# Kernel tuning notes

Measured on AMD Instinct MI355X. Metric: run time of the kernel, lower is better.

Reference implementation:

```python
import jax, jax.numpy as jnp
import numpy as np

NHEADS = 16
HEAD_DIM = 64
HIDDEN = 1024
QKV = NHEADS * HEAD_DIM  # 1024
SCALING = HEAD_DIM ** -0.5


def setup_inputs() -> dict:
    key = jax.random.key(0)
    k1, k2, k3, k4, k5 = jax.random.split(key, 5)
    B, S = 2, 2048
    hidden_states = jax.random.normal(k1, (B, S, HIDDEN), dtype=jnp.float32)
    # nn.Linear weights: stored [out, in]; kaiming-uniform-ish init scale
    w_qkv = jax.random.normal(k2, (3 * QKV, HIDDEN), dtype=jnp.float32) * (HIDDEN ** -0.5)
    b_qkv = jax.random.normal(k3, (3 * QKV,), dtype=jnp.float32) * 0.01
    w_o = jax.random.normal(k4, (HIDDEN, QKV), dtype=jnp.float32) * (QKV ** -0.5)
    b_o = jax.random.normal(k5, (HIDDEN,), dtype=jnp.float32) * 0.01
    return {"hidden_states": hidden_states, "w_qkv": w_qkv, "b_qkv": b_qkv,
            "w_o": w_o, "b_o": b_o}


def reference(hidden_states, w_qkv, b_qkv, w_o, b_o):
    B, S, _ = hidden_states.shape
    # qkv projection: x @ W^T + b  (torch nn.Linear convention)
    qkv = jnp.einsum('bsh,oh->bso', hidden_states, w_qkv) + b_qkv  # [B,S,3*QKV]
    xq, xk, xv = jnp.split(qkv, 3, axis=-1)
    # [B,S,H,D] -> [B,H,S,D]
    q = xq.reshape(B, S, NHEADS, HEAD_DIM).transpose(0, 2, 1, 3)
    k = xk.reshape(B, S, NHEADS, HEAD_DIM).transpose(0, 2, 1, 3)
    v = xv.reshape(B, S, NHEADS, HEAD_DIM).transpose(0, 2, 1, 3)
    scores = jnp.einsum('bhqd,bhkd->bhqk', q, k) * SCALING
    # dropout is identity in eval mode; mask is None in this config
    probs = jax.nn.softmax(scores.astype(jnp.float32), axis=-1).astype(q.dtype)
    out = jnp.einsum('bhqk,bhkd->bhqd', probs, v)  # [B,H,S,D]
    out = out.transpose(0, 2, 1, 3).reshape(B, S, QKV)
    return jnp.einsum('bsq,oq->bso', out, w_o) + b_o
```

## Files before the change

### kernel.cpp

```cpp
#include <hip/hip_runtime.h>

#define SEQ     2048
#define MROWS   4096
#define HID     1024
#define QKV3    3072
#define NH      16
#define HD      64
#define QSCALE  0.18033688f

typedef unsigned short u16;
typedef unsigned int   u32;
typedef __attribute__((ext_vector_type(8)))  short  bf16x8;
typedef __attribute__((ext_vector_type(4)))  float  floatx4;
typedef __attribute__((ext_vector_type(16))) float  floatx16;

__device__ __forceinline__ u16 f2bf(float f) {
    u32 u = __builtin_bit_cast(u32, f);
    u += 0x7fffu + ((u >> 16) & 1u);
    return (u16)(u >> 16);
}

#if __has_builtin(__builtin_amdgcn_cvt_pk_bf16_f32)
__device__ __forceinline__ ushort2 pack_bf(float a, float b) {
    auto r = __builtin_amdgcn_cvt_pk_bf16_f32(a, b);
    return __builtin_bit_cast(ushort2, r);
}
#else
__device__ __forceinline__ ushort2 pack_bf(float a, float b) {
    u32 ua = __builtin_bit_cast(u32, a) + 0x8000u;
    u32 ub = __builtin_bit_cast(u32, b) + 0x8000u;
    u32 d  = __builtin_amdgcn_perm(ub, ua, 0x07060302u);
    return __builtin_bit_cast(ushort2, d);
}
#endif

__device__ __forceinline__ void async_cp16(const void* g, void* l) {
    __builtin_amdgcn_global_load_lds(
        (const __attribute__((address_space(1))) unsigned int*)g,
        (__attribute__((address_space(3))) unsigned int*)l, 16, 0, 0);
}

#define N4_X   (MROWS * HID / 4)
#define N4_WQ  (QKV3 * HID / 4)
#define N4_WO  (HID * HID / 4)
__global__ void cvt_all(const float* __restrict__ x, const float* __restrict__ wq,
                        const float* __restrict__ wo, u16* __restrict__ xb,
                        u16* __restrict__ wqb, u16* __restrict__ wob) {
    int i = blockIdx.x * blockDim.x + threadIdx.x;
    const float* src; u16* dst; int k;
    if (i < N4_X)                { src = x;  dst = xb;  k = i; }
    else if (i < N4_X + N4_WQ)   { src = wq; dst = wqb; k = i - N4_X; }
    else                         { src = wo; dst = wob; k = i - N4_X - N4_WQ; }
    float4 v = ((const float4*)src)[k];
    ushort2 lo = pack_bf(v.x, v.y), hi = pack_bf(v.z, v.w);
    ushort4 o = {lo.x, lo.y, hi.x, hi.y};
    ((ushort4*)dst)[k] = o;
}

template <int MODE, int NT>
__global__ __launch_bounds__(256)
void gemm_bf16_nt(const u16* __restrict__ A, const u16* __restrict__ B,
                  const float* __restrict__ bias, float* __restrict__ Cout,
                  int M, int N, int K,
                  u16* __restrict__ q_ws, u16* __restrict__ k_ws,
                  u16* __restrict__ vt_ws) {
    constexpr int WN = NT / 2;
    constexpr int NJ = WN / 16;
    __shared__ u16 As[2][128 * 32];
    __shared__ u16 Bs[2][NT * 32];
    const int t  = (int)threadIdx.x;
    const int w  = t >> 6, l = t & 63;
    const int wr = w >> 1, wc = w & 1;
    const int m0 = (int)blockIdx.y * 128, n0 = (int)blockIdx.x * NT;
    const int lrow = l >> 2;
    const int lseg = ((l & 3) ^ ((l >> 3) & 3)) * 8;
    const int fm = l & 15, fq = l >> 4;
    const int fseg = (fq ^ ((fm >> 1) & 3)) * 8;

    auto stage = [&](int k0, int bb) {
#pragma unroll
        for (int rep = 0; rep < 2; ++rep) {
            const int chunk = w + rep * 4;
            const int row   = chunk * 16 + lrow;
            async_cp16(A + (size_t)(m0 + row) * K + k0 + lseg, &As[bb][chunk * 512]);
            if (NT == 128 || rep == 0)
                async_cp16(B + (size_t)(n0 + row) * K + k0 + lseg, &Bs[bb][chunk * 512]);
        }
    };

    floatx4 acc[4][NJ];
#pragma unroll
    for (int i = 0; i < 4; ++i)
#pragma unroll
        for (int j = 0; j < NJ; ++j) acc[i][j] = (floatx4)(0.f);

    const int T = K >> 5;
    stage(0, 0);
    for (int tt = 0; tt < T; ++tt) {
        const int cur = tt & 1;
        __syncthreads();
        if (tt + 1 < T) stage((tt + 1) << 5, cur ^ 1);
        bf16x8 af[4], bf[NJ];
#pragma unroll
        for (int i = 0; i < 4; ++i)
            af[i] = *(const bf16x8*)&As[cur][(wr * 64 + i * 16 + fm) * 32 + fseg];
#pragma unroll
        for (int j = 0; j < NJ; ++j)
            bf[j] = *(const bf16x8*)&Bs[cur][(wc * WN + j * 16 + fm) * 32 + fseg];
#pragma unroll
        for (int i = 0; i < 4; ++i)
#pragma unroll
            for (int j = 0; j < NJ; ++j)
                acc[i][j] = __builtin_amdgcn_mfma_f32_16x16x32_bf16(
                    af[i], bf[j], acc[i][j], 0, 0, 0);
    }

#pragma unroll
    for (int j = 0; j < NJ; ++j) {
        const int col = n0 + wc * WN + j * 16 + fm;
        const float bv = bias[col];
        const int region = col >> 10;
        const int hh = (col >> 6) & 15, d = col & 63;
#pragma unroll
        for (int i = 0; i < 4; ++i) {
            const int row0 = m0 + wr * 64 + i * 16 + fq * 4;
            if (MODE == 0) {
#pragma unroll
                for (int r = 0; r < 4; ++r)
                    Cout[(size_t)(row0 + r) * N + col] = acc[i][j][r] + bv;
            } else if (region < 2) {
                u16* __restrict__ dst = (region == 0) ? q_ws : k_ws;
                const float sc = (region == 0) ? QSCALE : 1.0f;
#pragma unroll
                for (int r = 0; r < 4; ++r) {
                    const int row = row0 + r;
                    const int b = row >> 11, s = row & 2047;
                    dst[((size_t)(b * NH + hh) * SEQ + s) * HD + d] =
                        f2bf((acc[i][j][r] + bv) * sc);
                }
            } else {
                const int b = row0 >> 11, s0 = row0 & 2047;
                ushort2 lo = pack_bf(acc[i][j][0] + bv, acc[i][j][1] + bv);
                ushort2 hi = pack_bf(acc[i][j][2] + bv, acc[i][j][3] + bv);
                ushort4 o = {lo.x, lo.y, hi.x, hi.y};
                *(ushort4*)&vt_ws[((size_t)(b * NH + hh) * HD + d) * SEQ + s0] = o;
            }
        }
    }
}

__global__ __launch_bounds__(256)
void attn_mfma(const u16* __restrict__ qw, const u16* __restrict__ kw,
               const u16* __restrict__ vtw, u16* __restrict__ attn) {
    __shared__ u16 Ks [2][64 * 64];
    __shared__ u16 Vts[2][64 * 64];
    __shared__ u16 Ps[4][32 * 66];

    const int bh   = (int)blockIdx.x;
    const int qblk = (int)blockIdx.y * 128;
    const int t = (int)threadIdx.x;
    const int w = t >> 6, l = t & 63;
    const int ln = l & 31, half = l >> 5;
    const int srow = l >> 3, sseg = l & 7;
    const size_t headSD = (size_t)bh * SEQ * HD;
    const size_t headDS = (size_t)bh * HD * SEQ;

    auto stage = [&](int kt, int bb) {
#pragma unroll
        for (int rep = 0; rep < 2; ++rep) {
            const int c = w + rep * 4;
            async_cp16(kw + headSD + (size_t)(kt * 64 + c * 8 + srow) * HD
                           + ((sseg ^ srow) * 8), &Ks[bb][c * 512]);
            async_cp16(vtw + headDS + (size_t)(c * 8 + srow) * SEQ + kt * 64
                           + ((sseg ^ srow) * 8), &Vts[bb][c * 512]);
        }
    };

    const int qrow = qblk + w * 32 + ln;
    bf16x8 qa[4];
#pragma unroll
    for (int kc = 0; kc < 4; ++kc)
        qa[kc] = *(const bf16x8*)(qw + headSD + (size_t)qrow * HD + kc * 16 + half * 8);

    floatx16 oacc[2];
    oacc[0] = (floatx16)(0.f); oacc[1] = (floatx16)(0.f);
    float2 ps2 = {0.f, 0.f};

    stage(0, 0);
    for (int kt = 0; kt < SEQ / 64; ++kt) {
        const int cur = kt & 1;
        __syncthreads();
        if (kt + 1 < SEQ / 64) stage(kt + 1, cur ^ 1);

        floatx16 sacc[2];
        sacc[0] = (floatx16)(0.f); sacc[1] = (floatx16)(0.f);
#pragma unroll
        for (int j = 0; j < 2; ++j) {
            const int krow = j * 32 + ln;
#pragma unroll
            for (int kc = 0; kc < 4; ++kc) {
                const int seg = (2 * kc + half) ^ (krow & 7);
                bf16x8 kb = *(const bf16x8*)&Ks[cur][krow * 64 + seg * 8];
                sacc[j] = __builtin_amdgcn_mfma_f32_32x32x16_bf16(kb, qa[kc], sacc[j], 0, 0, 0);
            }
        }

#pragma unroll
        for (int j = 0; j < 2; ++j) {
#pragma unroll
            for (int g = 0; g < 4; ++g) {
#pragma unroll
                for (int rp = 0; rp < 2; ++rp) {
                    const int r0 = 4 * g + 2 * rp;
                    const float p0 = exp2f(sacc[j][r0]);
                    const float p1 = exp2f(sacc[j][r0 + 1]);
                    ps2.x += p0; ps2.y += p1;
                    *(ushort2*)&Ps[w][ln * 66 + j * 32 + 8 * g + 4 * half + 2 * rp]
                        = pack_bf(p0, p1);
                }
            }
        }

#pragma unroll
        for (int kc = 0; kc < 4; ++kc) {
            bf16x8 pb = *(const bf16x8*)&Ps[w][ln * 66 + kc * 16 + half * 8];
#pragma unroll
            for (int n = 0; n < 2; ++n) {
                const int vrow = n * 32 + ln;
                const int seg = (2 * kc + half) ^ (vrow & 7);
                bf16x8 vb = *(const bf16x8*)&Vts[cur][vrow * 64 + seg * 8];
                oacc[n] = __builtin_amdgcn_mfma_f32_32x32x16_bf16(vb, pb, oacc[n], 0, 0, 0);
            }
        }
    }

    float psum = ps2.x + ps2.y;
    const float lsum = psum + __shfl_xor(psum, 32);
    const float inv  = 1.0f / lsum;

    const int b = bh >> 4, h = bh & 15;
    u16* __restrict__ orow =
        attn + (size_t)(b * SEQ + qblk + w * 32 + ln) * HID + h * HD;
#pragma unroll
    for (int n = 0; n < 2; ++n) {
#pragma unroll
        for (int g = 0; g < 4; ++g) {
#pragma unroll
            for (int rp = 0; rp < 2; ++rp) {
                const int r0 = 4 * g + 2 * rp;
                *(ushort2*)&orow[n * 32 + 8 * g + 4 * half + 2 * rp]
                    = pack_bf(oacc[n][r0] * inv, oacc[n][r0 + 1] * inv);
            }
        }
    }
}

extern "C" void kernel_launch(void* const* d_in, const int* in_sizes, int n_in,
                              void* d_out, int out_size, void* d_ws, size_t ws_size,
                              hipStream_t stream) {
    const float* x     = (const float*)d_in[0];
    const float* w_qkv = (const float*)d_in[1];
    const float* b_qkv = (const float*)d_in[2];
    const float* w_o   = (const float*)d_in[3];
    const float* b_o   = (const float*)d_in[4];
    float* outp = (float*)d_out;

    u16* xb    = (u16*)d_ws;
    u16* wqkvb = xb    + (size_t)MROWS * HID;
    u16* wob   = wqkvb + (size_t)QKV3 * HID;
    u16* q_ws  = wob   + (size_t)HID * HID;
    u16* k_ws  = q_ws  + (size_t)MROWS * HID;
    u16* vt_ws = k_ws  + (size_t)MROWS * HID;
    u16* attnb = vt_ws + (size_t)MROWS * HID;

    const int blk = 256;
    cvt_all<<<(N4_X + N4_WQ + N4_WO) / blk, blk, 0, stream>>>(
        x, w_qkv, w_o, xb, wqkvb, wob);

    gemm_bf16_nt<1, 128><<<dim3(QKV3 / 128, MROWS / 128), blk, 0, stream>>>(
        xb, wqkvb, b_qkv, nullptr, MROWS, QKV3, HID, q_ws, k_ws, vt_ws);

    attn_mfma<<<dim3(NH * 2, SEQ / 128), blk, 0, stream>>>(q_ws, k_ws, vt_ws, attnb);

    gemm_bf16_nt<0, 64><<<dim3(HID / 64, MROWS / 128), blk, 0, stream>>>(
        attnb, wob, b_o, outp, MROWS, HID, HID, nullptr, nullptr, nullptr);
}
```

Baseline: 202.9 us.

## Switch attention kernel to 16x16x32 MFMA with eight waves per block

The attention kernel moves from 32x32x16 MFMA tiles with 4 waves each owning 32 query rows to 16x16x32 MFMA tiles with 8 waves each owning 16 query rows, launched as 512-thread blocks. Each thread now issues a single async copy per stage instead of two, and the P staging buffer is re-laid out with padding of 72. The aim is more waves in flight to hide LDS and exp latency, with fewer accumulator registers per wave. The cost is more MFMA instructions per tile and K/V LDS reads amortised over fewer query rows per wave.

Result: no change. 201.0 us (-0.9%).

```diff
diff --git a/kernel.cpp b/kernel.cpp
--- a/kernel.cpp
+++ b/kernel.cpp
@@ -12,7 +12,6 @@
 typedef unsigned int   u32;
 typedef __attribute__((ext_vector_type(8)))  short  bf16x8;
 typedef __attribute__((ext_vector_type(4)))  float  floatx4;
-typedef __attribute__((ext_vector_type(16))) float  floatx16;
 
 __device__ __forceinline__ u16 f2bf(float f) {
     u32 u = __builtin_bit_cast(u32, f);
@@ -149,42 +148,39 @@
     }
 }
 
-__global__ __launch_bounds__(256)
+__global__ __launch_bounds__(512, 4)
 void attn_mfma(const u16* __restrict__ qw, const u16* __restrict__ kw,
                const u16* __restrict__ vtw, u16* __restrict__ attn) {
     __shared__ u16 Ks [2][64 * 64];
     __shared__ u16 Vts[2][64 * 64];
-    __shared__ u16 Ps[4][32 * 66];
+    __shared__ u16 Ps[8][16 * 72];
 
     const int bh   = (int)blockIdx.x;
     const int qblk = (int)blockIdx.y * 128;
     const int t = (int)threadIdx.x;
     const int w = t >> 6, l = t & 63;
-    const int ln = l & 31, half = l >> 5;
+    const int fm = l & 15, fq = l >> 4;
     const int srow = l >> 3, sseg = l & 7;
     const size_t headSD = (size_t)bh * SEQ * HD;
     const size_t headDS = (size_t)bh * HD * SEQ;
 
     auto stage = [&](int kt, int bb) {
-#pragma unroll
-        for (int rep = 0; rep < 2; ++rep) {
-            const int c = w + rep * 4;
-            async_cp16(kw + headSD + (size_t)(kt * 64 + c * 8 + srow) * HD
-                           + ((sseg ^ srow) * 8), &Ks[bb][c * 512]);
-            async_cp16(vtw + headDS + (size_t)(c * 8 + srow) * SEQ + kt * 64
-                           + ((sseg ^ srow) * 8), &Vts[bb][c * 512]);
-        }
+        async_cp16(kw + headSD + (size_t)(kt * 64 + w * 8 + srow) * HD
+                       + ((sseg ^ srow) * 8), &Ks[bb][w * 512]);
+        async_cp16(vtw + headDS + (size_t)(w * 8 + srow) * SEQ + kt * 64
+                       + ((sseg ^ srow) * 8), &Vts[bb][w * 512]);
     };
 
-    const int qrow = qblk + w * 32 + ln;
-    bf16x8 qa[4];
-#pragma unroll
-    for (int kc = 0; kc < 4; ++kc)
-        qa[kc] = *(const bf16x8*)(qw + headSD + (size_t)qrow * HD + kc * 16 + half * 8);
-
-    floatx16 oacc[2];
-    oacc[0] = (floatx16)(0.f); oacc[1] = (floatx16)(0.f);
-    float2 ps2 = {0.f, 0.f};
+    const int qrow = qblk + w * 16 + fm;
+    bf16x8 qa[2];
+#pragma unroll
+    for (int kc = 0; kc < 2; ++kc)
+        qa[kc] = *(const bf16x8*)(qw + headSD + (size_t)qrow * HD + kc * 32 + fq * 8);
+
+    floatx4 oacc[4];
+#pragma unroll
+    for (int dt = 0; dt < 4; ++dt) oacc[dt] = (floatx4)(0.f);
+    float psum = 0.f;
 
     stage(0, 0);
     for (int kt = 0; kt < SEQ / 64; ++kt) {
@@ -192,66 +188,53 @@
         __syncthreads();
         if (kt + 1 < SEQ / 64) stage(kt + 1, cur ^ 1);
 
-        floatx16 sacc[2];
-        sacc[0] = (floatx16)(0.f); sacc[1] = (floatx16)(0.f);
-#pragma unroll
-        for (int j = 0; j < 2; ++j) {
-            const int krow = j * 32 + ln;
-#pragma unroll
-            for (int kc = 0; kc < 4; ++kc) {
-                const int seg = (2 * kc + half) ^ (krow & 7);
-                bf16x8 kb = *(const bf16x8*)&Ks[cur][krow * 64 + seg * 8];
-                sacc[j] = __builtin_amdgcn_mfma_f32_32x32x16_bf16(kb, qa[kc], sacc[j], 0, 0, 0);
+        floatx4 sacc[4];
+#pragma unroll
+        for (int j = 0; j < 4; ++j) sacc[j] = (floatx4)(0.f);
+#pragma unroll
+        for (int j = 0; j < 4; ++j) {
+#pragma unroll
+            for (int kc = 0; kc < 2; ++kc) {
+                const int seg = (4 * kc + fq) ^ (fm & 7);
+                bf16x8 ka = *(const bf16x8*)&Ks[cur][(j * 16 + fm) * 64 + seg * 8];
+                sacc[j] = __builtin_amdgcn_mfma_f32_16x16x32_bf16(ka, qa[kc], sacc[j], 0, 0, 0);
             }
         }
 
 #pragma unroll
-        for (int j = 0; j < 2; ++j) {
-#pragma unroll
-            for (int g = 0; g < 4; ++g) {
-#pragma unroll
-                for (int rp = 0; rp < 2; ++rp) {
-                    const int r0 = 4 * g + 2 * rp;
-                    const float p0 = exp2f(sacc[j][r0]);
-                    const float p1 = exp2f(sacc[j][r0 + 1]);
-                    ps2.x += p0; ps2.y += p1;
-                    *(ushort2*)&Ps[w][ln * 66 + j * 32 + 8 * g + 4 * half + 2 * rp]
-                        = pack_bf(p0, p1);
-                }
+        for (int j = 0; j < 4; ++j) {
+            const float p0 = exp2f(sacc[j][0]);
+            const float p1 = exp2f(sacc[j][1]);
+            const float p2 = exp2f(sacc[j][2]);
+            const float p3 = exp2f(sacc[j][3]);
+            psum += (p0 + p1) + (p2 + p3);
+            *(ushort2*)&Ps[w][fm * 72 + j * 16 + fq * 4]     = pack_bf(p0, p1);
+            *(ushort2*)&Ps[w][fm * 72 + j * 16 + fq * 4 + 2] = pack_bf(p2, p3);
+        }
+
+#pragma unroll
+        for (int kc = 0; kc < 2; ++kc) {
+            bf16x8 pb = *(const bf16x8*)&Ps[w][fm * 72 + kc * 32 + fq * 8];
+#pragma unroll
+            for (int dt = 0; dt < 4; ++dt) {
+                const int seg = (4 * kc + fq) ^ (fm & 7);
+                bf16x8 va = *(const bf16x8*)&Vts[cur][(dt * 16 + fm) * 64 + seg * 8];
+                oacc[dt] = __builtin_amdgcn_mfma_f32_16x16x32_bf16(va, pb, oacc[dt], 0, 0, 0);
             }
         }
-
-#pragma unroll
-        for (int kc = 0; kc < 4; ++kc) {
-            bf16x8 pb = *(const bf16x8*)&Ps[w][ln * 66 + kc * 16 + half * 8];
-#pragma unroll
-            for (int n = 0; n < 2; ++n) {
-                const int vrow = n * 32 + ln;
-                const int seg = (2 * kc + half) ^ (vrow & 7);
-                bf16x8 vb = *(const bf16x8*)&Vts[cur][vrow * 64 + seg * 8];
-                oacc[n] = __builtin_amdgcn_mfma_f32_32x32x16_bf16(vb, pb, oacc[n], 0, 0, 0);
-            }
-        }
-    }
-
-    float psum = ps2.x + ps2.y;
-    const float lsum = psum + __shfl_xor(psum, 32);
-    const float inv  = 1.0f / lsum;
+    }
+
+    psum += __shfl_xor(psum, 16);
+    psum += __shfl_xor(psum, 32);
+    const float inv = 1.0f / psum;
 
     const int b = bh >> 4, h = bh & 15;
     u16* __restrict__ orow =
-        attn + (size_t)(b * SEQ + qblk + w * 32 + ln) * HID + h * HD;
-#pragma unroll
-    for (int n = 0; n < 2; ++n) {
-#pragma unroll
-        for (int g = 0; g < 4; ++g) {
-#pragma unroll
-            for (int rp = 0; rp < 2; ++rp) {
-                const int r0 = 4 * g + 2 * rp;
-                *(ushort2*)&orow[n * 32 + 8 * g + 4 * half + 2 * rp]
-                    = pack_bf(oacc[n][r0] * inv, oacc[n][r0 + 1] * inv);
-            }
-        }
+        attn + (size_t)(b * SEQ + qblk + w * 16 + fm) * HID + h * HD;
+#pragma unroll
+    for (int dt = 0; dt < 4; ++dt) {
+        *(ushort2*)&orow[dt * 16 + fq * 4]     = pack_bf(oacc[dt][0] * inv, oacc[dt][1] * inv);
+        *(ushort2*)&orow[dt * 16 + fq * 4 + 2] = pack_bf(oacc[dt][2] * inv, oacc[dt][3] * inv);
     }
 }
 
@@ -280,7 +263,7 @@
     gemm_bf16_nt<1, 128><<<dim3(QKV3 / 128, MROWS / 128), blk, 0, stream>>>(
         xb, wqkvb, b_qkv, nullptr, MROWS, QKV3, HID, q_ws, k_ws, vt_ws);
 
-    attn_mfma<<<dim3(NH * 2, SEQ / 128), blk, 0, stream>>>(q_ws, k_ws, vt_ws, attnb);
+    attn_mfma<<<dim3(NH * 2, SEQ / 128), 512, 0, stream>>>(q_ws, k_ws, vt_ws, attnb);
 
     gemm_bf16_nt<0, 64><<<dim3(HID / 64, MROWS / 128), blk, 0, stream>>>(
         attnb, wob, b_o, outp, MROWS, HID, HID, nullptr, nullptr, nullptr);
```
